# Kernel tuning notes

Measured on AMD Instinct MI355X. Metric: run time of the kernel, lower is better.

## Reference

```python
import jax, jax.numpy as jnp
import numpy as np

NUM_HEADS = 16
HEAD_DIM = 64
BSZ, SEQ, EMBED = 2, 2048, NUM_HEADS * HEAD_DIM
SCALE = HEAD_DIM ** (-0.5)
NEG = -1e9  # large negative for masked positions (finite, fp16-unsafe values avoided)


def setup_inputs() -> dict:
    key = jax.random.key(0)
    kq, kk, kv = jax.random.split(key, 3)
    q = jax.random.normal(kq, (BSZ, SEQ, EMBED), dtype=jnp.float32)
    k = jax.random.normal(kk, (BSZ, SEQ, EMBED), dtype=jnp.float32)
    v = jax.random.normal(kv, (BSZ, SEQ, EMBED), dtype=jnp.float32)
    # additive causal mask: 0 on/below diagonal, NEG above, shape (bsz,1,tgt,src)
    causal = jnp.where(jnp.tril(jnp.ones((SEQ, SEQ), dtype=bool)), 0.0, NEG).astype(jnp.float32)
    causal = jnp.broadcast_to(causal[None, None], (BSZ, 1, SEQ, SEQ))
    return {"query_states": q, "key_states": k, "value_states": v,
            "causal_attention_mask": causal}


def reference(query_states, key_states, value_states, causal_attention_mask):
    bsz, tgt_len, embed_dim = query_states.shape
    # [b, h, s, d]
    def shape_heads(t):
        return t.reshape(bsz, -1, NUM_HEADS, HEAD_DIM).transpose(0, 2, 1, 3)
    q = shape_heads(query_states * SCALE)
    k = shape_heads(key_states)
    v = shape_heads(value_states)
    # scores: [b, h, tgt, src]
    attn_weights = jnp.einsum('bhqd,bhkd->bhqk', q, k)
    attn_weights = attn_weights + causal_attention_mask  # broadcast over heads
    attn_probs = jax.nn.softmax(attn_weights, axis=-1)
    # dropout p=0.0 / eval mode -> identity
    attn_output = jnp.einsum('bhqk,bhkd->bhqd', attn_probs, v)
    attn_output = attn_output.transpose(0, 2, 1, 3).reshape(bsz, tgt_len, embed_dim)
    return attn_output
```

## Files before the change

### kernel.cpp

```cpp
#include <hip/hip_runtime.h>
#include <hip/hip_bf16.h>
#include <stdint.h>

#define BSZ 2
#define SEQ 2048
#define NHEADS 16
#define HDIM 64
#define EMBED (NHEADS * HDIM)
#define NQT 32

#define QSCALE 0.1803368801111244f
#define C2 11.5416914f

typedef unsigned short u16;
typedef unsigned int u32;
typedef __attribute__((ext_vector_type(8))) short bf16x8;
typedef __attribute__((ext_vector_type(16))) float f32x16;

#define TILE_B 8192
#define WSV_OFF (8ull * 1024 * 1024)

__device__ __forceinline__ u32 pkbf(float x, float y) {
  union { __hip_bfloat162 h; u32 u; } c;
  c.h = __float22bfloat162_rn(make_float2(x, y));
  return c.u;
}

__device__ __forceinline__ void gload16(const void* g, void* l) {
  __builtin_amdgcn_global_load_lds(
      (const __attribute__((address_space(1))) u32*)g,
      (__attribute__((address_space(3))) u32*)l, 16, 0, 0);
}

__global__ __launch_bounds__(256) void prep_kv(const float* __restrict__ K,
                                               const float* __restrict__ V,
                                               char* __restrict__ ws) {
  __shared__ float tile[64][68];
  if (blockIdx.x < 2048) {
    const int t = blockIdx.x * 256 + threadIdx.x;
    const int c = t & 7;
    const int h = (t >> 3) & 15;
    const size_t bs = (size_t)(t >> 7);
    const int s = (int)(bs & 2047);
    const int b = (int)(bs >> 11);
    const float* p = K + bs * EMBED + h * HDIM + c * 8;
    const float4 a = *reinterpret_cast<const float4*>(p);
    const float4 d = *reinterpret_cast<const float4*>(p + 4);
    uint4 out;
    out.x = pkbf(a.x, a.y); out.y = pkbf(a.z, a.w);
    out.z = pkbf(d.x, d.y); out.w = pkbf(d.z, d.w);
    const int kt = s >> 6, key = s & 63;
    const int kb = key >> 5;
    const int ks = c >> 1, hi = c & 1;
    const int lane = hi * 32 + (key & 31);
    char* dst = ws + ((size_t)(b * 16 + h) * 32 + kt) * TILE_B +
                ((kb * 4 + ks) * 64 + lane) * 16;
    *reinterpret_cast<uint4*>(dst) = out;
  } else {
    const int blk = blockIdx.x - 2048;
    const int kt = blk & 31, bh = blk >> 5;
    const int b = bh >> 4, h = bh & 15;
    const float* src = V + ((size_t)b * SEQ + kt * 64) * EMBED + h * HDIM;
    const int t = threadIdx.x;
    {
      const int row = t >> 2, c0 = (t & 3) * 16;
      const float* p = src + (size_t)row * EMBED + c0;
#pragma unroll
      for (int j = 0; j < 4; ++j)
        *reinterpret_cast<float4*>(&tile[row][c0 + 4 * j]) =
            *reinterpret_cast<const float4*>(p + 4 * j);
    }
    __syncthreads();
    const int d = t & 63;
#pragma unroll
    for (int halfc = 0; halfc < 2; ++halfc) {
      const int kc = (t >> 6) + halfc * 4;
      const int kb = kc >> 2, hi = kc & 1;
      const int ka0 = kc * 8;
      const int base = kb * 32 + (ka0 & 16) + hi * 4;
      uint4 out;
      out.x = pkbf(tile[base + 0][d], tile[base + 1][d]);
      out.y = pkbf(tile[base + 2][d], tile[base + 3][d]);
      out.z = pkbf(tile[base + 8][d], tile[base + 9][d]);
      out.w = pkbf(tile[base + 10][d], tile[base + 11][d]);
      const int lane = hi * 32 + (d & 31);
      const int db = d >> 5;
      const int ks2 = (kc >> 1) & 1;
      char* dst = ws + WSV_OFF + ((size_t)bh * 32 + kt) * TILE_B +
                  ((kb * 4 + ks2 * 2 + db) * 64 + lane) * 16;
      *reinterpret_cast<uint4*>(dst) = out;
    }
  }
}

__device__ __forceinline__ void stream_step(const char* Kc, const char* Vc,
                                            const bf16x8 q0, const bf16x8 q1,
                                            const bf16x8 q2, const bf16x8 q3,
                                            f32x16& o0, f32x16& o1, float& lsum,
                                            int kb, int l, int lq, int hi,
                                            bool diagq) {
  f32x16 s = {};
  __builtin_amdgcn_s_setprio(1);
  {
    const bf16x8 kf0 = *reinterpret_cast<const bf16x8*>(Kc + ((kb * 4 + 0) * 64 + l) * 16);
    s = __builtin_amdgcn_mfma_f32_32x32x16_bf16(kf0, q0, s, 0, 0, 0);
    const bf16x8 kf1 = *reinterpret_cast<const bf16x8*>(Kc + ((kb * 4 + 1) * 64 + l) * 16);
    s = __builtin_amdgcn_mfma_f32_32x32x16_bf16(kf1, q1, s, 0, 0, 0);
    const bf16x8 kf2 = *reinterpret_cast<const bf16x8*>(Kc + ((kb * 4 + 2) * 64 + l) * 16);
    s = __builtin_amdgcn_mfma_f32_32x32x16_bf16(kf2, q2, s, 0, 0, 0);
    const bf16x8 kf3 = *reinterpret_cast<const bf16x8*>(Kc + ((kb * 4 + 3) * 64 + l) * 16);
    s = __builtin_amdgcn_mfma_f32_32x32x16_bf16(kf3, q3, s, 0, 0, 0);
  }
  __builtin_amdgcn_s_setprio(0);

  if (diagq) {
#pragma unroll
    for (int r = 0; r < 16; ++r) {
      const int crow = (r & 3) + 8 * (r >> 2) + 4 * hi;
      if (crow > lq) s[r] = -1.0e30f;
    }
  }

  float e[16];
#pragma unroll
  for (int r = 0; r < 16; ++r) e[r] = __builtin_amdgcn_exp2f(s[r] - C2);
  lsum += ((e[0] + e[1]) + (e[2] + e[3])) + ((e[4] + e[5]) + (e[6] + e[7])) +
          ((e[8] + e[9]) + (e[10] + e[11])) + ((e[12] + e[13]) + (e[14] + e[15]));
  union { u32 w[4]; bf16x8 v; } pa0, pa1;
#pragma unroll
  for (int i = 0; i < 4; ++i) {
    pa0.w[i] = pkbf(e[2 * i], e[2 * i + 1]);
    pa1.w[i] = pkbf(e[8 + 2 * i], e[8 + 2 * i + 1]);
  }

  __builtin_amdgcn_s_setprio(1);
  {
    const bf16x8 v00 = *reinterpret_cast<const bf16x8*>(Vc + ((kb * 4 + 0) * 64 + l) * 16);
    o0 = __builtin_amdgcn_mfma_f32_32x32x16_bf16(pa0.v, v00, o0, 0, 0, 0);
    const bf16x8 v01 = *reinterpret_cast<const bf16x8*>(Vc + ((kb * 4 + 1) * 64 + l) * 16);
    o1 = __builtin_amdgcn_mfma_f32_32x32x16_bf16(pa0.v, v01, o1, 0, 0, 0);
    const bf16x8 v10 = *reinterpret_cast<const bf16x8*>(Vc + ((kb * 4 + 2) * 64 + l) * 16);
    o0 = __builtin_amdgcn_mfma_f32_32x32x16_bf16(pa1.v, v10, o0, 0, 0, 0);
    const bf16x8 v11 = *reinterpret_cast<const bf16x8*>(Vc + ((kb * 4 + 3) * 64 + l) * 16);
    o1 = __builtin_amdgcn_mfma_f32_32x32x16_bf16(pa1.v, v11, o1, 0, 0, 0);
  }
  __builtin_amdgcn_s_setprio(0);
}

__device__ __forceinline__ void write_stream(float* __restrict__ O, int b, int h,
                                             int qt, int qhalf, int lq, int hi,
                                             int l, const f32x16& o0,
                                             const f32x16& o1,
                                             const float* __restrict__ Obuf,
                                             float linv) {
  float* outg = O + ((size_t)b * SEQ + qt * 64 + qhalf * 32) * EMBED + h * HDIM;
#pragma unroll
  for (int r = 0; r < 16; ++r) {
    const int crow = (r & 3) + 8 * (r >> 2) + 4 * hi;
    const float il = __shfl(linv, crow, 64);
    const float v0 = (o0[r] + Obuf[r * 64 + l]) * il;
    const float v1 = (o1[r] + Obuf[1024 + r * 64 + l]) * il;
    outg[(size_t)crow * EMBED + lq] = v0;
    outg[(size_t)crow * EMBED + 32 + lq] = v1;
  }
}

__global__ __launch_bounds__(256, 2) void mha_fwd(const float* __restrict__ Q,
                                                  const char* __restrict__ ws,
                                                  float* __restrict__ O) {
  __shared__ __align__(16) char smem[33280];

  const int id = ((blockIdx.x & 7) << 6) | (blockIdx.x >> 3);
  const int qlo = id & 15, bh = id >> 4;
  const int qhi = (NQT - 1) - qlo;
  const int b = bh >> 4, h = bh & 15;

  const int wv = threadIdx.x >> 6;
  const int l = threadIdx.x & 63;
  const int qhalf = wv & 1, kb = wv >> 1;
  const int lq = l & 31;
  const int hi = l >> 5;

  bf16x8 qh[4], ql[4];
  {
    union { uint4 u; bf16x8 v; } cv;
#pragma unroll
    for (int st = 0; st < 2; ++st) {
      const int qt = st ? qlo : qhi;
      const float* qp =
          Q + ((size_t)b * SEQ + qt * 64 + qhalf * 32 + lq) * EMBED + h * HDIM + hi * 8;
#pragma unroll
      for (int ks = 0; ks < 4; ++ks) {
        const float4 a = *reinterpret_cast<const float4*>(qp + ks * 16);
        const float4 d = *reinterpret_cast<const float4*>(qp + ks * 16 + 4);
        cv.u.x = pkbf(a.x * QSCALE, a.y * QSCALE);
        cv.u.y = pkbf(a.z * QSCALE, a.w * QSCALE);
        cv.u.z = pkbf(d.x * QSCALE, d.y * QSCALE);
        cv.u.w = pkbf(d.z * QSCALE, d.w * QSCALE);
        if (st) ql[ks] = cv.v; else qh[ks] = cv.v;
      }
    }
  }

  const char* gK = ws + (size_t)bh * 32 * TILE_B;
  const char* gV = ws + WSV_OFF + (size_t)bh * 32 * TILE_B;

#define STAGE(dstoff, src)                                                    \
  {                                                                           \
    const char* s_ = (src);                                                   \
    gload16(s_ + wv * 2048 + l * 16, smem + (dstoff) + wv * 2048);            \
    gload16(s_ + wv * 2048 + 1024 + l * 16, smem + (dstoff) + wv * 2048 + 1024); \
  }

  STAGE(0, gK);
  STAGE(16384, gV);
  __syncthreads();

  f32x16 oh0 = {}, oh1 = {}, ol0 = {}, ol1 = {};
  float lsh = 0.f, lsl = 0.f;

  int cur = 0;
  for (int kt = 0; kt <= qhi; ++kt) {
    const bool more = kt < qhi;
    if (more) {
      STAGE((cur ^ 1) * 8192, gK + (size_t)(kt + 1) * TILE_B);
      STAGE(16384 + (cur ^ 1) * 8192, gV + (size_t)(kt + 1) * TILE_B);
    }
    const char* Kc = smem + cur * 8192;
    const char* Vc = smem + 16384 + cur * 8192;

    {
      const bool diag = (kt == qhi);
      if (!(diag && kb == 1 && qhalf == 0))
        stream_step(Kc, Vc, qh[0], qh[1], qh[2], qh[3], oh0, oh1, lsh,
                    kb, l, lq, hi, diag && (kb == qhalf));
    }
    if (kt <= qlo) {
      const bool diag = (kt == qlo);
      if (!(diag && kb == 1 && qhalf == 0))
        stream_step(Kc, Vc, ql[0], ql[1], ql[2], ql[3], ol0, ol1, lsl,
                    kb, l, lq, hi, diag && (kb == qhalf));
    }

    if (more) __syncthreads();
    cur ^= 1;
  }

  __syncthreads();
  const float l2h = lsh + __shfl_xor(lsh, 32, 64);
  const float l2l = lsl + __shfl_xor(lsl, 32, 64);
  float* Obuf = reinterpret_cast<float*>(smem);
  float* Lbuf = reinterpret_cast<float*>(smem + 32768);

  if (kb == 1) {
#pragma unroll
    for (int r = 0; r < 16; ++r) {
      Obuf[(qhalf * 2 + 0) * 1024 + r * 64 + l] = oh0[r];
      Obuf[(qhalf * 2 + 1) * 1024 + r * 64 + l] = oh1[r];
      Obuf[((2 + qhalf) * 2 + 0) * 1024 + r * 64 + l] = ol0[r];
      Obuf[((2 + qhalf) * 2 + 1) * 1024 + r * 64 + l] = ol1[r];
    }
    if (l < 32) {
      Lbuf[qhalf * 32 + lq] = l2h;
      Lbuf[(2 + qhalf) * 32 + lq] = l2l;
    }
  }
  __syncthreads();
  if (kb == 0) {
    const float linv_h = 1.0f / (l2h + Lbuf[qhalf * 32 + lq]);
    write_stream(O, b, h, qhi, qhalf, lq, hi, l, oh0, oh1,
                 Obuf + (qhalf * 2) * 1024, linv_h);
    const float linv_l = 1.0f / (l2l + Lbuf[(2 + qhalf) * 32 + lq]);
    write_stream(O, b, h, qlo, qhalf, lq, hi, l, ol0, ol1,
                 Obuf + ((2 + qhalf) * 2) * 1024, linv_l);
  }
#undef STAGE
}

extern "C" void kernel_launch(void* const* d_in, const int* in_sizes, int n_in,
                              void* d_out, int out_size, void* d_ws, size_t ws_size,
                              hipStream_t stream) {
  const float* q = (const float*)d_in[0];
  const float* k = (const float*)d_in[1];
  const float* v = (const float*)d_in[2];
  float* o = (float*)d_out;
  char* ws = (char*)d_ws;

  prep_kv<<<dim3(3072), dim3(256), 0, stream>>>(k, v, ws);
  mha_fwd<<<dim3(512), dim3(256), 0, stream>>>(q, ws, o);
}
```

Before: 50.59 us.

## Load K/V fragments straight from global into registers with double-buffering

```diff
diff --git a/kernel.cpp b/kernel.cpp
--- a/kernel.cpp
+++ b/kernel.cpp
@@ -24,12 +24,6 @@
   union { __hip_bfloat162 h; u32 u; } c;
   c.h = __float22bfloat162_rn(make_float2(x, y));
   return c.u;
-}
-
-__device__ __forceinline__ void gload16(const void* g, void* l) {
-  __builtin_amdgcn_global_load_lds(
-      (const __attribute__((address_space(1))) u32*)g,
-      (__attribute__((address_space(3))) u32*)l, 16, 0, 0);
 }
 
 __global__ __launch_bounds__(256) void prep_kv(const float* __restrict__ K,
@@ -93,24 +87,17 @@
   }
 }
 
-__device__ __forceinline__ void stream_step(const char* Kc, const char* Vc,
-                                            const bf16x8 q0, const bf16x8 q1,
-                                            const bf16x8 q2, const bf16x8 q3,
-                                            f32x16& o0, f32x16& o1, float& lsum,
-                                            int kb, int l, int lq, int hi,
-                                            bool diagq) {
+__device__ __forceinline__ void stream_step_r(const bf16x8* kf, const bf16x8* vf,
+                                              const bf16x8 q0, const bf16x8 q1,
+                                              const bf16x8 q2, const bf16x8 q3,
+                                              f32x16& o0, f32x16& o1, float& lsum,
+                                              int l, int lq, int hi, bool diagq) {
   f32x16 s = {};
   __builtin_amdgcn_s_setprio(1);
-  {
-    const bf16x8 kf0 = *reinterpret_cast<const bf16x8*>(Kc + ((kb * 4 + 0) * 64 + l) * 16);
-    s = __builtin_amdgcn_mfma_f32_32x32x16_bf16(kf0, q0, s, 0, 0, 0);
-    const bf16x8 kf1 = *reinterpret_cast<const bf16x8*>(Kc + ((kb * 4 + 1) * 64 + l) * 16);
-    s = __builtin_amdgcn_mfma_f32_32x32x16_bf16(kf1, q1, s, 0, 0, 0);
-    const bf16x8 kf2 = *reinterpret_cast<const bf16x8*>(Kc + ((kb * 4 + 2) * 64 + l) * 16);
-    s = __builtin_amdgcn_mfma_f32_32x32x16_bf16(kf2, q2, s, 0, 0, 0);
-    const bf16x8 kf3 = *reinterpret_cast<const bf16x8*>(Kc + ((kb * 4 + 3) * 64 + l) * 16);
-    s = __builtin_amdgcn_mfma_f32_32x32x16_bf16(kf3, q3, s, 0, 0, 0);
-  }
+  s = __builtin_amdgcn_mfma_f32_32x32x16_bf16(kf[0], q0, s, 0, 0, 0);
+  s = __builtin_amdgcn_mfma_f32_32x32x16_bf16(kf[1], q1, s, 0, 0, 0);
+  s = __builtin_amdgcn_mfma_f32_32x32x16_bf16(kf[2], q2, s, 0, 0, 0);
+  s = __builtin_amdgcn_mfma_f32_32x32x16_bf16(kf[3], q3, s, 0, 0, 0);
   __builtin_amdgcn_s_setprio(0);
 
   if (diagq) {
@@ -134,16 +121,10 @@
   }
 
   __builtin_amdgcn_s_setprio(1);
-  {
-    const bf16x8 v00 = *reinterpret_cast<const bf16x8*>(Vc + ((kb * 4 + 0) * 64 + l) * 16);
-    o0 = __builtin_amdgcn_mfma_f32_32x32x16_bf16(pa0.v, v00, o0, 0, 0, 0);
-    const bf16x8 v01 = *reinterpret_cast<const bf16x8*>(Vc + ((kb * 4 + 1) * 64 + l) * 16);
-    o1 = __builtin_amdgcn_mfma_f32_32x32x16_bf16(pa0.v, v01, o1, 0, 0, 0);
-    const bf16x8 v10 = *reinterpret_cast<const bf16x8*>(Vc + ((kb * 4 + 2) * 64 + l) * 16);
-    o0 = __builtin_amdgcn_mfma_f32_32x32x16_bf16(pa1.v, v10, o0, 0, 0, 0);
-    const bf16x8 v11 = *reinterpret_cast<const bf16x8*>(Vc + ((kb * 4 + 3) * 64 + l) * 16);
-    o1 = __builtin_amdgcn_mfma_f32_32x32x16_bf16(pa1.v, v11, o1, 0, 0, 0);
-  }
+  o0 = __builtin_amdgcn_mfma_f32_32x32x16_bf16(pa0.v, vf[0], o0, 0, 0, 0);
+  o1 = __builtin_amdgcn_mfma_f32_32x32x16_bf16(pa0.v, vf[1], o1, 0, 0, 0);
+  o0 = __builtin_amdgcn_mfma_f32_32x32x16_bf16(pa1.v, vf[2], o0, 0, 0, 0);
+  o1 = __builtin_amdgcn_mfma_f32_32x32x16_bf16(pa1.v, vf[3], o1, 0, 0, 0);
   __builtin_amdgcn_s_setprio(0);
 }
 
@@ -168,7 +149,7 @@
 __global__ __launch_bounds__(256, 2) void mha_fwd(const float* __restrict__ Q,
                                                   const char* __restrict__ ws,
                                                   float* __restrict__ O) {
-  __shared__ __align__(16) char smem[33280];
+  __shared__ __align__(16) float Obuf[8 * 1024 + 128];
 
   const int id = ((blockIdx.x & 7) << 6) | (blockIdx.x >> 3);
   const int qlo = id & 15, bh = id >> 4;
@@ -202,55 +183,52 @@
     }
   }
 
-  const char* gK = ws + (size_t)bh * 32 * TILE_B;
-  const char* gV = ws + WSV_OFF + (size_t)bh * 32 * TILE_B;
-
-#define STAGE(dstoff, src)                                                    \
+  const char* gKw = ws + (size_t)bh * 32 * TILE_B + kb * 4096 + l * 16;
+  const char* gVw = ws + WSV_OFF + (size_t)bh * 32 * TILE_B + kb * 4096 + l * 16;
+
+#define LOADF(kf, vf, t_)                                                     \
   {                                                                           \
-    const char* s_ = (src);                                                   \
-    gload16(s_ + wv * 2048 + l * 16, smem + (dstoff) + wv * 2048);            \
-    gload16(s_ + wv * 2048 + 1024 + l * 16, smem + (dstoff) + wv * 2048 + 1024); \
-  }
-
-  STAGE(0, gK);
-  STAGE(16384, gV);
-  __syncthreads();
+    const char* pK = gKw + (size_t)(t_) * TILE_B;                             \
+    const char* pV = gVw + (size_t)(t_) * TILE_B;                             \
+    kf[0] = *reinterpret_cast<const bf16x8*>(pK);                             \
+    kf[1] = *reinterpret_cast<const bf16x8*>(pK + 1024);                      \
+    kf[2] = *reinterpret_cast<const bf16x8*>(pK + 2048);                      \
+    kf[3] = *reinterpret_cast<const bf16x8*>(pK + 3072);                      \
+    vf[0] = *reinterpret_cast<const bf16x8*>(pV);                             \
+    vf[1] = *reinterpret_cast<const bf16x8*>(pV + 1024);                      \
+    vf[2] = *reinterpret_cast<const bf16x8*>(pV + 2048);                      \
+    vf[3] = *reinterpret_cast<const bf16x8*>(pV + 3072);                      \
+  }
 
   f32x16 oh0 = {}, oh1 = {}, ol0 = {}, ol1 = {};
   float lsh = 0.f, lsl = 0.f;
 
-  int cur = 0;
-  for (int kt = 0; kt <= qhi; ++kt) {
-    const bool more = kt < qhi;
-    if (more) {
-      STAGE((cur ^ 1) * 8192, gK + (size_t)(kt + 1) * TILE_B);
-      STAGE(16384 + (cur ^ 1) * 8192, gV + (size_t)(kt + 1) * TILE_B);
-    }
-    const char* Kc = smem + cur * 8192;
-    const char* Vc = smem + 16384 + cur * 8192;
-
-    {
-      const bool diag = (kt == qhi);
-      if (!(diag && kb == 1 && qhalf == 0))
-        stream_step(Kc, Vc, qh[0], qh[1], qh[2], qh[3], oh0, oh1, lsh,
-                    kb, l, lq, hi, diag && (kb == qhalf));
-    }
-    if (kt <= qlo) {
-      const bool diag = (kt == qlo);
-      if (!(diag && kb == 1 && qhalf == 0))
-        stream_step(Kc, Vc, ql[0], ql[1], ql[2], ql[3], ol0, ol1, lsl,
-                    kb, l, lq, hi, diag && (kb == qhalf));
-    }
-
-    if (more) __syncthreads();
-    cur ^= 1;
-  }
-
-  __syncthreads();
+#define PROC(kf, vf, t_)                                                      \
+  {                                                                           \
+    const int t = (t_);                                                       \
+    const bool dh = (t == qhi), dl = (t == qlo);                              \
+    if (!(dh && kb == 1 && qhalf == 0))                                       \
+      stream_step_r(kf, vf, qh[0], qh[1], qh[2], qh[3], oh0, oh1, lsh,        \
+                    l, lq, hi, dh && (kb == qhalf));                          \
+    if ((t <= qlo) && !(dl && kb == 1 && qhalf == 0))                         \
+      stream_step_r(kf, vf, ql[0], ql[1], ql[2], ql[3], ol0, ol1, lsl,        \
+                    l, lq, hi, dl && (kb == qhalf));                          \
+  }
+
+  bf16x8 kfA[4], vfA[4], kfB[4], vfB[4];
+  LOADF(kfA, vfA, 0);
+  int kt = 0;
+  for (; kt + 1 <= qhi; kt += 2) {
+    LOADF(kfB, vfB, kt + 1);
+    PROC(kfA, vfA, kt);
+    if (kt + 2 <= qhi) LOADF(kfA, vfA, kt + 2);
+    PROC(kfB, vfB, kt + 1);
+  }
+  if (kt <= qhi) PROC(kfA, vfA, kt);
+
   const float l2h = lsh + __shfl_xor(lsh, 32, 64);
   const float l2l = lsl + __shfl_xor(lsl, 32, 64);
-  float* Obuf = reinterpret_cast<float*>(smem);
-  float* Lbuf = reinterpret_cast<float*>(smem + 32768);
+  float* Lbuf = Obuf + 8 * 1024;
 
   if (kb == 1) {
 #pragma unroll
@@ -274,7 +252,8 @@
     write_stream(O, b, h, qlo, qhalf, lq, hi, l, ol0, ol1,
                  Obuf + ((2 + qhalf) * 2) * 1024, linv_l);
   }
-#undef STAGE
+#undef LOADF
+#undef PROC
 }
 
 extern "C" void kernel_launch(void* const* d_in, const int* in_sizes, int n_in,
```

Result: faster. 47.88 us (median of 3 runs) (-5.4%).
